# Kernel optimization log

Hardware: AMD Instinct MI355X
Metric: run time of the kernel (lower is better)

The kernel has to match this reference:

```python
import jax, jax.numpy as jnp
import numpy as np
import math

LMAX = 3
NUM_LAYERS = 2
MUL = 32
AVG_NEIGH = 16.0
CUTOFF = 2.5
P_ENV = 6
N_RB = 8

# ---------- real Clebsch-Gordan (Wigner 3j) coefficients ----------

def _su2_cg(j1, j2, j3, m1, m2, m3):
    if m1 + m2 != m3:
        return 0.0
    f = math.factorial
    pref = math.sqrt((2 * j3 + 1) * f(j1 + j2 - j3) * f(j1 - j2 + j3) * f(-j1 + j2 + j3) / f(j1 + j2 + j3 + 1)
                     * f(j3 + m3) * f(j3 - m3) * f(j1 - m1) * f(j1 + m1) * f(j2 - m2) * f(j2 + m2))
    s = 0.0
    kmin = max(0, j2 - j3 - m1, j1 - j3 + m2)
    kmax = min(j1 + j2 - j3, j1 - m1, j2 + m2)
    for k in range(kmin, kmax + 1):
        s += (-1.0) ** k / (f(k) * f(j1 + j2 - j3 - k) * f(j1 - m1 - k) * f(j2 + m2 - k)
                            * f(j3 - j2 + m1 + k) * f(j3 - j1 - m2 + k))
    return pref * s

def _q_real_to_complex(l):
    q = np.zeros((2 * l + 1, 2 * l + 1), dtype=np.complex128)
    for m in range(-l, 0):
        q[l + m, l + abs(m)] = 1 / np.sqrt(2)
        q[l + m, l - abs(m)] = -1j / np.sqrt(2)
    q[l, l] = 1.0
    for m in range(1, l + 1):
        q[l + m, l + abs(m)] = (-1) ** m / np.sqrt(2)
        q[l + m, l - abs(m)] = 1j * (-1) ** m / np.sqrt(2)
    return (-1j) ** l * q

def _real_cg(l1, l2, l3):
    C = np.zeros((2 * l1 + 1, 2 * l2 + 1, 2 * l3 + 1), dtype=np.complex128)
    for m1 in range(-l1, l1 + 1):
        for m2 in range(-l2, l2 + 1):
            m3 = m1 + m2
            if abs(m3) <= l3:
                C[l1 + m1, l2 + m2, l3 + m3] = _su2_cg(l1, l2, l3, m1, m2, m3)
    Q1, Q2, Q3 = _q_real_to_complex(l1), _q_real_to_complex(l2), _q_real_to_complex(l3)
    C = np.einsum('ia,jb,kc,abc->ijk', Q1, Q2, np.conj(Q3), C)
    Cr, Ci = np.real(C), np.imag(C)
    C = Cr if np.linalg.norm(Cr) >= np.linalg.norm(Ci) else Ci
    return (C / np.linalg.norm(C)).astype(np.float32)  # unit-norm invariant coupling tensor

W3J = {}
for _l1 in range(LMAX + 1):
    for _l2 in range(LMAX + 1):
        for _l3 in range(LMAX + 1):
            if abs(_l1 - _l2) <= _l3 <= _l1 + _l2:
                W3J[(_l1, _l2, _l3)] = jnp.asarray(_real_cg(_l1, _l2, _l3))

# ---------- spherical harmonics (component normalization, l=0..3) ----------

def _sh(u):
    x, y, z = u[:, 0], u[:, 1], u[:, 2]
    s3, s5, s15 = math.sqrt(3.0), math.sqrt(5.0), math.sqrt(15.0)
    sh0 = jnp.ones_like(x)[:, None]
    sh1 = s3 * jnp.stack([y, z, x], -1)
    sh2 = jnp.stack([s15 * x * y, s15 * y * z, 0.5 * s5 * (3 * z * z - 1.0),
                     s15 * x * z, 0.5 * s15 * (x * x - y * y)], -1)
    c1, c2, c3, c4 = math.sqrt(35.0 / 8.0), math.sqrt(105.0), math.sqrt(21.0 / 8.0), 0.5 * math.sqrt(7.0)
    sh3 = jnp.stack([c1 * y * (3 * x * x - y * y), c2 * x * y * z, c3 * y * (5 * z * z - 1.0),
                     c4 * z * (5 * z * z - 3.0), c3 * x * (5 * z * z - 1.0),
                     0.5 * c2 * z * (x * x - y * y), c1 * x * (x * x - 3 * y * y)], -1)
    return [sh0, sh1, sh2, sh3]

def _mlp(x, Ws):
    # e3nn-style MLP: no biases, 1/sqrt(fan_in) normalization, silu, linear last layer
    for i, W in enumerate(Ws):
        x = x @ (W / jnp.sqrt(1.0 * W.shape[0]))
        if i + 1 < len(Ws):
            x = jax.nn.silu(x)
    return x

def _envelope(x):
    p = P_ENV
    e = (1.0 - 0.5 * (p + 1) * (p + 2) * x ** p + p * (p + 2) * x ** (p + 1)
         - 0.5 * p * (p + 1) * x ** (p + 2))
    return jnp.where(x < 1.0, e, 0.0)

def _forward(node_attrs, vectors, we0, we1, winit, wenv, wlat0, wlat1, wmix, wout, senders, receivers):
    N = node_attrs.shape[0]
    E = vectors.shape[0]
    d = jnp.linalg.norm(vectors, axis=-1)                      # [E]
    uvec = vectors / (d[:, None] + 1e-9)                       # unit edge vectors
    dc = d / CUTOFF                                            # normalized distance in [0, inf)
    freqs = np.pi * np.arange(1, N_RB + 1, dtype=np.float32)
    rb = math.sqrt(2.0) * jnp.sin(dc[:, None] * freqs) / (dc[:, None] + 1e-9)  # [E, 8] Bessel basis
    cut = _envelope(dc)[:, None]                               # [E, 1] polynomial cutoff u(d, p)
    # two-body embedding: radial basis + sender/receiver species
    x = jnp.concatenate([rb, node_attrs[senders], node_attrs[receivers]], axis=-1)
    x = _mlp(x, [we0, we1]) * cut                              # [E, H]
    Y = _sh(uvec)                                              # list of [E, 2l+1]
    wi = (x @ (winit / jnp.sqrt(1.0 * winit.shape[0]))).reshape(E, LMAX + 1, MUL)
    V = [wi[:, l, :, None] * Y[l][:, None, :] for l in range(LMAX + 1)]  # [E, MUL, 2l+1]
    for layer in range(NUM_LAYERS):
        w = x @ (wenv[layer] / jnp.sqrt(1.0 * wenv.shape[1]))  # [E, MUL] env weights
        env = []
        for l in range(LMAX + 1):
            # environment embedding: scatter weighted SH onto nodes, gather back onto edges
            node_env = jax.ops.segment_sum(w[:, :, None] * Y[l][:, None, :], receivers, num_segments=N)
            env.append(node_env[senders] / jnp.sqrt(AVG_NEIGH))
        # equivariant CG tensor product env (x) V -> T, per output l3
        T = []
        for l3 in range(LMAX + 1):
            acc = None
            n = 0
            for l1 in range(LMAX + 1):
                for l2 in range(LMAX + 1):
                    if (l1, l2, l3) in W3J:
                        t = jnp.einsum('ijk,emi,emj->emk', W3J[(l1, l2, l3)], env[l1], V[l2])
                        acc = t if acc is None else acc + t
                        n += 1
            T.append(acc / np.sqrt(n))
        # scalars feed the latent track; latent MLP gated by cutoff
        x = jnp.concatenate([x, T[0][:, :, 0]], axis=-1)       # [E, H+MUL]
        x = _mlp(x, [wlat0[layer], wlat1[layer]]) * cut        # [E, H]
        # per-l channel mixing (e3nn Linear)
        V = [jnp.einsum('emk,mn->enk', T[l], wmix[layer, l] / jnp.sqrt(1.0 * MUL)) for l in range(LMAX + 1)]
    # output head: 0e per-edge scalar
    return x @ (wout / jnp.sqrt(1.0 * wout.shape[0]))          # [E, 1]

def setup_inputs():
    key = jax.random.key(0)
    ks = jax.random.split(key, 12)
    N, E, S, H = 4096, 65536, 16, 512
    L = NUM_LAYERS
    return {
        'node_attrs': jax.random.normal(ks[0], (N, S), jnp.float32),
        'vectors': jax.random.normal(ks[1], (E, 3), jnp.float32),
        'we0': jax.random.normal(ks[2], (N_RB + 2 * S, H), jnp.float32),
        'we1': jax.random.normal(ks[3], (H, H), jnp.float32),
        'winit': jax.random.normal(ks[4], (H, (LMAX + 1) * MUL), jnp.float32),
        'wenv': jax.random.normal(ks[5], (L, H, MUL), jnp.float32),
        'wlat0': jax.random.normal(ks[6], (L, H + MUL, H), jnp.float32),
        'wlat1': jax.random.normal(ks[7], (L, H, H), jnp.float32),
        'wmix': jax.random.normal(ks[8], (L, LMAX + 1, MUL, MUL), jnp.float32),
        'wout': jax.random.normal(ks[9], (H, 1), jnp.float32),
        'senders': jax.random.randint(ks[10], (E,), 0, N, jnp.int32),
        'receivers': jax.random.randint(ks[11], (E,), 0, N, jnp.int32),
    }

def reference(node_attrs, vectors, we0, we1, winit, wenv, wlat0, wlat1, wmix, wout, senders, receivers):
    return _forward(node_attrs, vectors, we0, we1, winit, wenv, wlat0, wlat1, wmix, wout, senders, receivers)
```

## Files before the change

### kernel.cpp

```cpp
#include <hip/hip_runtime.h>
#include <math.h>
#include <type_traits>

typedef __attribute__((ext_vector_type(8))) short s8v;
typedef __attribute__((ext_vector_type(4))) float f4v;
typedef __attribute__((ext_vector_type(2))) float f2v;

#define CH 8192

__device__ inline float b2f(unsigned short u){ return __uint_as_float(((unsigned)u)<<16); }
__device__ inline unsigned short f2b(float f){
  unsigned u = __float_as_uint(f);
  return (unsigned short)((u + 0x7FFFu + ((u>>16)&1u)) >> 16);
}
__device__ inline void stC(float* p, float v){ *p = v; }
__device__ inline void stC(unsigned short* p, float v){ *p = f2b(v); }

__device__ __forceinline__ void gl16(const void* g, void* l){
  __builtin_amdgcn_global_load_lds(
      (const __attribute__((address_space(1))) unsigned*)g,
      (__attribute__((address_space(3))) unsigned*)l, 16, 0, 0);
}

constexpr double FCT[11] = {1.,1.,2.,6.,24.,120.,720.,5040.,40320.,362880.,3628800.};
constexpr double csqrt_c(double x){
  double g = x > 1.0 ? x : 1.0;
  for (int i=0;i<60;i++) g = 0.5*(g + x/g);
  return g;
}
struct CD { double re, im; };
constexpr CD cmulc(CD a, CD b){ return {a.re*b.re - a.im*b.im, a.re*b.im + a.im*b.re}; }

constexpr double su2cg_c(int j1,int j2,int j3,int m1,int m2,int m3){
  if (m1+m2 != m3) return 0.0;
  double pref = csqrt_c((double)(2*j3+1) * FCT[j1+j2-j3]*FCT[j1-j2+j3]*FCT[-j1+j2+j3]/FCT[j1+j2+j3+1]
              * FCT[j3+m3]*FCT[j3-m3]*FCT[j1-m1]*FCT[j1+m1]*FCT[j2-m2]*FCT[j2+m2]);
  int kmin = 0;
  if (j2-j3-m1 > kmin) kmin = j2-j3-m1;
  if (j1-j3+m2 > kmin) kmin = j1-j3+m2;
  int kmax = j1+j2-j3;
  if (j1-m1 < kmax) kmax = j1-m1;
  if (j2+m2 < kmax) kmax = j2+m2;
  double s = 0.0;
  for (int k=kmin;k<=kmax;k++){
    double t = 1.0/(FCT[k]*FCT[j1+j2-j3-k]*FCT[j1-m1-k]*FCT[j2+m2-k]*FCT[j3-j2+m1+k]*FCT[j3-j1-m2+k]);
    s += (k&1) ? -t : t;
  }
  return pref*s;
}

constexpr CD qelem_c(int l, int i, int j){
  int m = i - l;
  const double is2 = 0.70710678118654752440;
  double re=0.0, im=0.0;
  if (m < 0){
    if (j == l - m) re = is2;
    else if (j == l + m) im = -is2;
  } else if (m == 0){
    if (j == l) re = 1.0;
  } else {
    double sgn = (m & 1) ? -1.0 : 1.0;
    if (j == l + m) re = sgn*is2;
    else if (j == l - m) im = sgn*is2;
  }
  CD r{};
  switch (l & 3){
    case 0: r = {re, im}; break;
    case 1: r = {im, -re}; break;
    case 2: r = {-re, -im}; break;
    default: r = {-im, re}; break;
  }
  return r;
}

constexpr double TN3[4] = {0.5, 1.0/3.0, 0.30151134457776363, 0.31622776601683794};

template<int L1,int L2,int L3>
struct TriVals { float v[(2*L1+1)*(2*L2+1)*(2*L3+1)]; };

template<int L1,int L2,int L3>
constexpr TriVals<L1,L2,L3> make_tri(){
  constexpr int n1=2*L1+1, n2=2*L2+1, n3=2*L3+1;
  double cg[n1*n2*n3] = {};
  for (int a=0;a<n1;a++)
    for (int b=0;b<n2;b++)
      for (int c=0;c<n3;c++)
        cg[(a*n2+b)*n3+c] = su2cg_c(L1,L2,L3, a-L1, b-L2, c-L3);
  double cr[n1*n2*n3] = {};
  double ci[n1*n2*n3] = {};
  for (int i=0;i<n1;i++)
   for (int j=0;j<n2;j++)
    for (int k=0;k<n3;k++){
      double sre=0.0, sim=0.0;
      for (int a=0;a<n1;a++){
        CD q1 = qelem_c(L1,i,a);
        if (q1.re==0.0 && q1.im==0.0) continue;
        for (int b=0;b<n2;b++){
          CD q2 = qelem_c(L2,j,b);
          if (q2.re==0.0 && q2.im==0.0) continue;
          CD q12 = cmulc(q1,q2);
          for (int c=0;c<n3;c++){
            double g = cg[(a*n2+b)*n3+c];
            if (g == 0.0) continue;
            CD q3 = qelem_c(L3,k,c);
            CD q3c{q3.re, -q3.im};
            CD q = cmulc(q12,q3c);
            sre += q.re*g; sim += q.im*g;
          }
        }
      }
      cr[(i*n2+j)*n3+k]=sre; ci[(i*n2+j)*n3+k]=sim;
    }
  double nr=0.0, ni=0.0;
  for (int i=0;i<n1*n2*n3;i++){ nr += cr[i]*cr[i]; ni += ci[i]*ci[i]; }
  bool pr = nr >= ni;
  double nn = csqrt_c(pr ? nr : ni);
  TriVals<L1,L2,L3> t{};
  for (int i=0;i<n1*n2*n3;i++)
    t.v[i] = (float)(((pr ? cr[i] : ci[i]) / nn) * TN3[L3]);
  return t;
}

template<int L1,int L2,int L3>
constexpr TriVals<L1,L2,L3> W3V = make_tri<L1,L2,L3>();

constexpr int LOFFC[4] = {0,1,4,9};

template<int WB>
__device__ __forceinline__ void fmac_lit(float& a, float p){
  asm("v_fmac_f32 %0, %2, %1" : "+v"(a) : "v"(p), "i"(WB));
}

template<int I, int N, typename F>
__device__ __forceinline__ void sfor(F&& f){
  if constexpr (I < N){
    f(std::integral_constant<int,I>{});
    sfor<I+1,N>(static_cast<F&&>(f));
  }
}

template<int L1,int L2>
__device__ __forceinline__ void tp_pair(const float* __restrict__ env,
                                        const float* __restrict__ v,
                                        float* __restrict__ acc){
  sfor<0,2*L1+1>([&](auto K1c){
    constexpr int k1 = decltype(K1c)::value;
    sfor<0,2*L2+1>([&](auto K2c){
      constexpr int k2 = decltype(K2c)::value;
      float p = env[LOFFC[L1]+k1] * v[LOFFC[L2]+k2];
      sfor<0,4>([&](auto L3c){
        constexpr int l3 = decltype(L3c)::value;
        constexpr int lo = (L1>L2)?(L1-L2):(L2-L1);
        if constexpr (l3 >= lo && l3 <= L1+L2){
          sfor<0,2*l3+1>([&](auto K3c){
            constexpr int k3 = decltype(K3c)::value;
            constexpr float w = W3V<L1,L2,l3>.v[(k1*(2*L2+1)+k2)*(2*l3+1)+k3];
            if constexpr (w != 0.f){
              fmac_lit<__builtin_bit_cast(int, w)>(acc[LOFFC[l3]+k3], p);
            }
          });
        }
      });
    });
  });
}

template<int L1,int L2,int L3>
__device__ __forceinline__ void tp_tri(const float* __restrict__ env,
                                       const float* __restrict__ v,
                                       float* __restrict__ acc){
  constexpr int n1=2*L1+1, n2=2*L2+1, n3=2*L3+1;
  #pragma unroll
  for (int k1=0;k1<n1;k1++)
    #pragma unroll
    for (int k2=0;k2<n2;k2++){
      float p = env[LOFFC[L1]+k1] * v[LOFFC[L2]+k2];
      #pragma unroll
      for (int k3=0;k3<n3;k3++){
        float w = W3V<L1,L2,L3>.v[(k1*n2+k2)*n3+k3];
        if (w != 0.f) acc[LOFFC[L3]+k3] += w * p;
      }
    }
}

struct WSeg { const float* W; unsigned short* WT; int K, N, Kpad, nblk; };
struct WDesc { WSeg s[9]; };
__global__ __launch_bounds__(256) void wconv_all(WDesc d){
  int b = blockIdx.x;
  int seg = 0;
  while (b >= d.s[seg].nblk){ b -= d.s[seg].nblk; ++seg; }
  const WSeg w = d.s[seg];
  int idx = b*256 + threadIdx.x;
  if (idx >= w.N*w.Kpad) return;
  int n = idx / w.Kpad, k = idx - n*w.Kpad;
  w.WT[idx] = (k < w.K) ? f2b(w.W[(size_t)k*w.N + n]) : (unsigned short)0;
}

__global__ __launch_bounds__(256) void edge_init(
    const float* __restrict__ vec, const float* __restrict__ na,
    const int* __restrict__ snd, const int* __restrict__ rcv,
    unsigned short* __restrict__ feat, float* __restrict__ Y, float* __restrict__ cutb, int E)
{
  int e = blockIdx.x*256 + threadIdx.x;
  if (e >= E) return;
  float vx = vec[(size_t)e*3], vy = vec[(size_t)e*3+1], vz = vec[(size_t)e*3+2];
  float d = sqrtf(vx*vx + vy*vy + vz*vz);
  float inv = 1.f/(d + 1e-9f);
  float x = vx*inv, y = vy*inv, z = vz*inv;
  float dc = d * 0.4f;
  float dci = 1.f/(dc + 1e-9f);
  unsigned short* f = feat + (size_t)e*64;
  #pragma unroll
  for (int k=1;k<=8;k++)
    f[k-1] = f2b(1.41421356237309515f * sinf(dc * 3.14159265358979323846f * k) * dci);
  int s = snd[e], r = rcv[e];
  #pragma unroll
  for (int i=0;i<16;i++) f[8+i]  = f2b(na[(size_t)s*16+i]);
  #pragma unroll
  for (int i=0;i<16;i++) f[24+i] = f2b(na[(size_t)r*16+i]);
  #pragma unroll
  for (int i=40;i<64;i++) f[i] = 0;
  float cv = 0.f;
  if (dc < 1.f){
    float d2 = dc*dc; float d6 = d2*d2*d2; float d7 = d6*dc; float d8 = d7*dc;
    cv = 1.f - 28.f*d6 + 48.f*d7 - 21.f*d8;
  }
  cutb[e] = cv;
  float* Ye = Y + (size_t)e*16;
  const float s3=1.7320508075688772f, s5=2.2360679774997896f, s15=3.8729833462074170f;
  Ye[0] = 1.f;
  Ye[1] = s3*y; Ye[2] = s3*z; Ye[3] = s3*x;
  Ye[4] = s15*x*y; Ye[5] = s15*y*z; Ye[6] = 0.5f*s5*(3.f*z*z-1.f);
  Ye[7] = s15*x*z; Ye[8] = 0.5f*s15*(x*x - y*y);
  const float c1=2.0916500663351889f, c2=10.246950765959598f, c3=1.6201851746019649f, c4=1.3228756555322954f;
  Ye[9]  = c1*y*(3.f*x*x - y*y);
  Ye[10] = c2*x*y*z;
  Ye[11] = c3*y*(5.f*z*z - 1.f);
  Ye[12] = c4*z*(5.f*z*z - 3.f);
  Ye[13] = c3*x*(5.f*z*z - 1.f);
  Ye[14] = 0.5f*c2*z*(x*x - y*y);
  Ye[15] = c1*x*(x*x - 3.f*y*y);
}

template<int NT, typename TC, bool SILU, bool CUT, bool HASA2>
__global__ __launch_bounds__(256) void gemm_mfma(
    const unsigned short* __restrict__ A, int lda, int K1,
    const float* __restrict__ A2, int lda2,
    const unsigned short* __restrict__ WT, int ldw,
    TC* __restrict__ C, int ldc,
    const float* __restrict__ cutv,
    int N, int K, float scale)
{
  constexpr int NB = NT/16;
  __shared__ s8v As8[128*8];
  __shared__ s8v Bs8[NT*8];
  const int tid = threadIdx.x;
  const int wid = tid >> 6, lane = tid & 63;
  const int r15 = lane & 15, kg = lane >> 4;
  const int col0 = blockIdx.x * NT;
  const int row0 = blockIdx.y * 128;
  f4v acc[2][NB] = {};

  auto compute = [&](){
    #pragma unroll
    for (int s = 0; s < 2; s++) {
      const int cb = s*4 + kg;
      const int cx = cb ^ (r15 & 7);
      s8v a0 = As8[(wid*32      + r15)*8 + cx];
      s8v a1 = As8[(wid*32 + 16 + r15)*8 + cx];
      #pragma unroll
      for (int j = 0; j < NB; j++) {
        s8v b = Bs8[(j*16 + r15)*8 + cx];
        acc[0][j] = __builtin_amdgcn_mfma_f32_16x16x32_bf16(a0, b, acc[0][j], 0,0,0);
        acc[1][j] = __builtin_amdgcn_mfma_f32_16x16x32_bf16(a1, b, acc[1][j], 0,0,0);
      }
    }
  };

  const int Kfull = HASA2 ? K1 : K;
  for (int k0 = 0; k0 < Kfull; k0 += 64) {
    #pragma unroll
    for (int i = 0; i < 4; i++) {
      int seg = i*256 + tid;
      int r = seg >> 3, ks = seg & 7;
      int ksx = ks ^ (r & 7);
      gl16(A + (size_t)(row0+r)*lda + k0 + ksx*8, &As8[i*256 + (tid & ~63)]);
    }
    #pragma unroll
    for (int i = 0; i < NT/32; i++) {
      int seg = i*256 + tid;
      int n = seg >> 3, ks = seg & 7;
      int ksx = ks ^ (n & 7);
      gl16(WT + (size_t)(col0+n)*ldw + k0 + ksx*8, &Bs8[i*256 + (tid & ~63)]);
    }
    __syncthreads();
    compute();
    __syncthreads();
  }
  if (HASA2 && Kfull < K) {
    #pragma unroll
    for (int i = 0; i < 4; i++) {
      int seg = i*256 + tid;
      int r = seg >> 3, ks = seg & 7;
      int cl = ks ^ (r & 7);
      s8v val = {};
      #pragma unroll
      for (int j = 0; j < 8; j++) {
        int kk = cl*8 + j;
        if (K1 + kk < K) val[j] = (short)f2b(A2[(size_t)(row0+r)*lda2 + kk]);
      }
      As8[seg] = val;
    }
    #pragma unroll
    for (int i = 0; i < NT/32; i++) {
      int seg = i*256 + tid;
      int n = seg >> 3, ks = seg & 7;
      int ksx = ks ^ (n & 7);
      gl16(WT + (size_t)(col0+n)*ldw + K1 + ksx*8, &Bs8[i*256 + (tid & ~63)]);
    }
    __syncthreads();
    compute();
  }
  #pragma unroll
  for (int g=0; g<2; g++) {
    #pragma unroll
    for (int c=0; c<NB; c++) {
      int col = col0 + c*16 + r15;
      if (col >= N) continue;
      #pragma unroll
      for (int j=0;j<4;j++) {
        int row = row0 + wid*32 + g*16 + kg*4 + j;
        float v = acc[g][c][j] * scale;
        if (SILU) v = v / (1.f + __expf(-v));
        if (CUT)  v *= cutv[row];
        stC(&C[(size_t)row*ldc + col], v);
      }
    }
  }
}

__global__ __launch_bounds__(256) void vbuild(
    const unsigned short* __restrict__ wi, const float* __restrict__ Y,
    unsigned short* __restrict__ V, int count)
{
  int t = blockIdx.x*256 + threadIdx.x;
  if (t >= count*32) return;
  int e = t >> 5, m = t & 31;
  const unsigned short* wr = wi + (size_t)e*128 + m;
  float ws[4] = { b2f(wr[0]), b2f(wr[32]), b2f(wr[64]), b2f(wr[96]) };
  const float4* Y4 = (const float4*)(Y + (size_t)e*16);
  float yv[16];
  #pragma unroll
  for (int q=0;q<4;q++){ float4 f=Y4[q]; yv[q*4]=f.x; yv[q*4+1]=f.y; yv[q*4+2]=f.z; yv[q*4+3]=f.w; }
  constexpr int LOFK[16] = {0,1,1,1,2,2,2,2,2,3,3,3,3,3,3,3};
  s8v o0, o1;
  #pragma unroll
  for (int k=0;k<8;k++)  o0[k] = (short)f2b(ws[LOFK[k]]   * yv[k]);
  #pragma unroll
  for (int k=0;k<8;k++)  o1[k] = (short)f2b(ws[LOFK[8+k]] * yv[8+k]);
  s8v* vo = (s8v*)(V + (size_t)e*512 + (size_t)m*16);
  vo[0] = o0; vo[1] = o1;
}

__global__ __launch_bounds__(256) void hist_k(
    const int* __restrict__ rcv, int* __restrict__ deg, int E)
{
  int e = blockIdx.x*256 + threadIdx.x;
  if (e < E) atomicAdd(&deg[rcv[e]], 1);
}

__global__ __launch_bounds__(256) void scan_k(
    const int* __restrict__ deg, int* __restrict__ offs, int Nn)
{
  __shared__ int part[256];
  const int t = threadIdx.x;
  const int per = (Nn + 255) / 256;
  int base = t*per;
  int loc[32];
  int s = 0;
  for (int i=0;i<per;i++){ int v = (base+i<Nn)?deg[base+i]:0; loc[i]=s; s+=v; }
  part[t] = s;
  __syncthreads();
  for (int off=1; off<256; off<<=1){
    int v = (t>=off) ? part[t-off] : 0;
    __syncthreads();
    part[t] += v;
    __syncthreads();
  }
  int pre = (t==0) ? 0 : part[t-1];
  for (int i=0;i<per;i++) if (base+i<Nn) offs[base+i] = pre + loc[i];
  if (t==255) offs[Nn] = part[255];
}

__global__ __launch_bounds__(256) void fill_k(
    const int* __restrict__ rcv, int* __restrict__ cursor,
    const int* __restrict__ offs, int* __restrict__ elist, int E)
{
  int e = blockIdx.x*256 + threadIdx.x;
  if (e >= E) return;
  int r = rcv[e];
  int p = atomicAdd(&cursor[r], 1);
  elist[offs[r] + p] = e;
}

__global__ __launch_bounds__(512) void env_build(
    const float* __restrict__ w, const float* __restrict__ Y,
    const int* __restrict__ elist, const int* __restrict__ offs,
    float* __restrict__ nenv)
{
  const int n = blockIdx.x;
  const int j = threadIdx.x;
  const int m = j >> 4, kk = j & 15;
  const int beg = offs[n], end = offs[n+1];
  float acc = 0.f;
  for (int p = beg; p < end; ++p) {
    int e = elist[p];
    acc += w[(size_t)e*32 + m] * Y[(size_t)e*16 + kk];
  }
  nenv[(size_t)n*512 + j] = acc;
}

__global__ __launch_bounds__(256, 2) void tp_mix(
    const float* __restrict__ nenv, const int* __restrict__ senders,
    unsigned short* __restrict__ V,
    const float* __restrict__ wm,
    float* __restrict__ t0, int E)
{
  __shared__ float Ts[8][32][18];
  const int tid = threadIdx.x;
  const int le = tid >> 5, m = tid & 31;
  const int e = blockIdx.x*8 + le;
  const int s = senders[e];
  float env[16], v[16], acc[16];
  const float4* ne4 = (const float4*)(nenv + (size_t)s*512 + (size_t)m*16);
  #pragma unroll
  for (int q=0;q<4;q++){
    float4 f = ne4[q];
    env[q*4]=f.x; env[q*4+1]=f.y; env[q*4+2]=f.z; env[q*4+3]=f.w;
  }
  const s8v* vv = (const s8v*)(V + (size_t)e*512 + (size_t)m*16);
  s8v v0 = vv[0], v1 = vv[1];
  #pragma unroll
  for (int q=0;q<8;q++){ v[q] = b2f((unsigned short)v0[q]); v[8+q] = b2f((unsigned short)v1[q]); }
  #pragma unroll
  for (int k=0;k<16;k++) acc[k] = 0.f;

  tp_pair<0,0>(env,v,acc); tp_pair<0,1>(env,v,acc); tp_pair<0,2>(env,v,acc); tp_pair<0,3>(env,v,acc);
  tp_pair<1,0>(env,v,acc); tp_pair<1,1>(env,v,acc); tp_pair<1,2>(env,v,acc); tp_pair<1,3>(env,v,acc);
  tp_pair<2,0>(env,v,acc); tp_pair<2,1>(env,v,acc); tp_pair<2,2>(env,v,acc); tp_pair<2,3>(env,v,acc);
  tp_pair<3,0>(env,v,acc); tp_pair<3,1>(env,v,acc); tp_pair<3,2>(env,v,acc); tp_pair<3,3>(env,v,acc);

  t0[(size_t)e*32 + m] = acc[0];

  #pragma unroll
  for (int k=0;k<16;k++) Ts[le][m][k] = acc[k];
  __syncthreads();
  f2v o2[8];
  #pragma unroll
  for (int kp=0;kp<8;kp++){ o2[kp][0]=0.f; o2[kp][1]=0.f; }
  #pragma unroll
  for (int mm=0; mm<32; mm++) {
    float w0 = wm[        mm*32 + m];
    float w1 = wm[1024 +  mm*32 + m];
    float w2 = wm[2048 +  mm*32 + m];
    float w3 = wm[3072 +  mm*32 + m];
    const f2v* tr = (const f2v*)Ts[le][mm];
    f2v p01; p01[0]=w0; p01[1]=w1;
    f2v p11; p11[0]=w1; p11[1]=w1;
    f2v p22; p22[0]=w2; p22[1]=w2;
    f2v p23; p23[0]=w2; p23[1]=w3;
    f2v p33; p33[0]=w3; p33[1]=w3;
    o2[0] += tr[0]*p01; o2[1] += tr[1]*p11; o2[2] += tr[2]*p22; o2[3] += tr[3]*p22;
    o2[4] += tr[4]*p23; o2[5] += tr[5]*p33; o2[6] += tr[6]*p33; o2[7] += tr[7]*p33;
  }
  s8v oa, ob;
  #pragma unroll
  for (int kp=0;kp<4;kp++){
    oa[2*kp]   = (short)f2b(o2[kp][0]   * 0.17677669529663689f);
    oa[2*kp+1] = (short)f2b(o2[kp][1]   * 0.17677669529663689f);
    ob[2*kp]   = (short)f2b(o2[4+kp][0] * 0.17677669529663689f);
    ob[2*kp+1] = (short)f2b(o2[4+kp][1] * 0.17677669529663689f);
  }
  s8v* vo = (s8v*)(V + (size_t)e*512 + (size_t)m*16);
  vo[0] = oa; vo[1] = ob;
}

__global__ __launch_bounds__(256) void tp_last(
    const float* __restrict__ nenv, const int* __restrict__ senders,
    const unsigned short* __restrict__ V, float* __restrict__ t0, int E)
{
  int t = blockIdx.x*256 + threadIdx.x;
  int e = t >> 5, m = t & 31;
  if (e >= E) return;
  int s = senders[e];
  float env[16], v[16], acc[16];
  const float4* ne4 = (const float4*)(nenv + (size_t)s*512 + (size_t)m*16);
  #pragma unroll
  for (int q=0;q<4;q++){
    float4 f = ne4[q];
    env[q*4]=f.x; env[q*4+1]=f.y; env[q*4+2]=f.z; env[q*4+3]=f.w;
  }
  const s8v* vv = (const s8v*)(V + (size_t)e*512 + (size_t)m*16);
  s8v v0 = vv[0], v1 = vv[1];
  #pragma unroll
  for (int q=0;q<8;q++){ v[q] = b2f((unsigned short)v0[q]); v[8+q] = b2f((unsigned short)v1[q]); }
  #pragma unroll
  for (int k=0;k<16;k++) acc[k] = 0.f;
  tp_tri<0,0,0>(env,v,acc); tp_tri<1,1,0>(env,v,acc);
  tp_tri<2,2,0>(env,v,acc); tp_tri<3,3,0>(env,v,acc);
  t0[(size_t)e*32 + m] = acc[0];
}

__global__ __launch_bounds__(256) void out_kernel(
    const unsigned short* __restrict__ x, const float* __restrict__ wout,
    float* __restrict__ out, int E)
{
  int gw = (blockIdx.x*256 + threadIdx.x) >> 6;
  int lane = threadIdx.x & 63;
  if (gw >= E) return;
  const s8v* xr = (const s8v*)(x + (size_t)gw*512);
  s8v chunk = xr[lane];
  float s = 0.f;
  #pragma unroll
  for (int j=0;j<8;j++) s += b2f((unsigned short)chunk[j]) * wout[lane*8 + j];
  #pragma unroll
  for (int off=32; off; off>>=1) s += __shfl_down(s, off);
  if (lane == 0) out[gw] = s * 0.044194173824159216f;
}

static inline size_t alup(size_t b){ return (b + 255) & ~(size_t)255; }
static size_t need_bytes(int E, int N, int chd){
  size_t s = 0;
  s += alup((size_t)E*16*4);
  s += alup((size_t)E*4);
  s += alup((size_t)E*32*4);
  s += alup((size_t)E*32*4);
  s += alup((size_t)N*512*4);
  s += alup((size_t)E*64*2);
  s += alup((size_t)chd*512*2);
  s += alup((size_t)E*512*2);
  s += alup((size_t)E*512*2);
  s += alup((size_t)512*64*2);
  s += alup((size_t)512*512*2);
  s += alup((size_t)128*512*2);
  s += alup((size_t)2*32*512*2);
  s += alup((size_t)2*512*544*2);
  s += alup((size_t)2*512*512*2);
  s += alup((size_t)N*4);
  s += alup(((size_t)N+1)*4);
  s += alup((size_t)N*4);
  s += alup((size_t)E*4);
  return s;
}

extern "C" void kernel_launch(void* const* d_in, const int* in_sizes, int n_in,
                              void* d_out, int out_size, void* d_ws, size_t ws_size,
                              hipStream_t stream)
{
  const float* node_attrs = (const float*)d_in[0];
  const float* vectors    = (const float*)d_in[1];
  const float* we0        = (const float*)d_in[2];
  const float* we1        = (const float*)d_in[3];
  const float* winit      = (const float*)d_in[4];
  const float* wenv       = (const float*)d_in[5];
  const float* wlat0      = (const float*)d_in[6];
  const float* wlat1      = (const float*)d_in[7];
  const float* wmix       = (const float*)d_in[8];
  const float* wout       = (const float*)d_in[9];
  const int*   senders    = (const int*)d_in[10];
  const int*   receivers  = (const int*)d_in[11];
  float* out = (float*)d_out;
  const int E = in_sizes[1] / 3;
  const int N = in_sizes[0] / 16;

  int CHD = -1;
  const int tiers[4] = {E, E/2, E/4, CH};
  for (int i=0;i<4;i++){
    if (tiers[i] >= CH && need_bytes(E, N, tiers[i]) <= ws_size){ CHD = tiers[i]; break; }
  }
  if (CHD < 0) return;

  char* base = (char*)d_ws;
  size_t off = 0;
  auto carve = [&](size_t b) -> char* { char* p = base + off; off += alup(b); return p; };
  float*          Yb    = (float*)carve((size_t)E*16*4);
  float*          cutb  = (float*)carve((size_t)E*4);
  float*          wbuf  = (float*)carve((size_t)E*32*4);
  float*          t0b   = (float*)carve((size_t)E*32*4);
  float*          nenv  = (float*)carve((size_t)N*512*4);
  unsigned short* feat  = (unsigned short*)carve((size_t)E*64*2);
  unsigned short* cbuf  = (unsigned short*)carve((size_t)CHD*512*2);
  unsigned short* Vb    = (unsigned short*)carve((size_t)E*512*2);
  unsigned short* xb    = (unsigned short*)carve((size_t)E*512*2);
  unsigned short* we0T  = (unsigned short*)carve((size_t)512*64*2);
  unsigned short* we1T  = (unsigned short*)carve((size_t)512*512*2);
  unsigned short* winT  = (unsigned short*)carve((size_t)128*512*2);
  unsigned short* wenvT = (unsigned short*)carve((size_t)2*32*512*2);
  unsigned short* wl0T  = (unsigned short*)carve((size_t)2*512*544*2);
  unsigned short* wl1T  = (unsigned short*)carve((size_t)2*512*512*2);
  int*            deg   = (int*)carve((size_t)N*4);
  int*            offs  = (int*)carve(((size_t)N+1)*4);
  int*            cursor= (int*)carve((size_t)N*4);
  int*            elist = (int*)carve((size_t)E*4);

  const float rs40  = 0.15811388300841897f;
  const float rs512 = 0.044194173824159216f;
  const float rs544 = 0.042874646285627205f;

  dim3 blk(256);
  WDesc wd;
  auto seg = [&](int i, const float* W, unsigned short* WT, int K, int Nn, int Kpad){
    wd.s[i] = { W, WT, K, Nn, Kpad, (Nn*Kpad + 255)/256 };
  };
  seg(0, we0,  we0T, 40, 512, 64);
  seg(1, we1,  we1T, 512, 512, 512);
  seg(2, winit, winT, 512, 128, 512);
  seg(3, wenv,                wenvT,            512, 32, 512);
  seg(4, wenv + (size_t)512*32, wenvT + (size_t)32*512, 512, 32, 512);
  seg(5, wlat0,                 wl0T,                 544, 512, 544);
  seg(6, wlat0 + (size_t)544*512, wl0T + (size_t)512*544, 544, 512, 544);
  seg(7, wlat1,                 wl1T,                 512, 512, 512);
  seg(8, wlat1 + (size_t)512*512, wl1T + (size_t)512*512, 512, 512, 512);
  int totblk = 0;
  for (int i=0;i<9;i++) totblk += wd.s[i].nblk;
  wconv_all<<<totblk, blk, 0, stream>>>(wd);

  edge_init<<<E/256, blk, 0, stream>>>(vectors, node_attrs, senders, receivers, feat, Yb, cutb, E);

  hipMemsetAsync(deg, 0, (size_t)N*4, stream);
  hipMemsetAsync(cursor, 0, (size_t)N*4, stream);
  hist_k<<<(E+255)/256, blk, 0, stream>>>(receivers, deg, E);
  scan_k<<<1, blk, 0, stream>>>(deg, offs, N);
  fill_k<<<(E+255)/256, blk, 0, stream>>>(receivers, cursor, offs, elist, E);

  for (int c0 = 0; c0 < E; c0 += CHD) {
    gemm_mfma<128,unsigned short,true,false,false><<<dim3(4, CHD/128), blk, 0, stream>>>(
        feat + (size_t)c0*64, 64, 64, nullptr, 0, we0T, 64, cbuf, 512, nullptr, 512, 64, rs40);
    gemm_mfma<128,unsigned short,false,true,false><<<dim3(4, CHD/128), blk, 0, stream>>>(
        cbuf, 512, 512, nullptr, 0, we1T, 512, xb + (size_t)c0*512, 512, cutb + c0, 512, 512, rs512);
    gemm_mfma<128,unsigned short,false,false,false><<<dim3(1, CHD/128), blk, 0, stream>>>(
        xb + (size_t)c0*512, 512, 512, nullptr, 0, winT, 512, cbuf, 128, nullptr, 128, 512, rs512);
    vbuild<<<(CHD*32)/256, blk, 0, stream>>>(cbuf, Yb + (size_t)c0*16, Vb + (size_t)c0*512, CHD);
  }

  for (int layer = 0; layer < 2; ++layer) {
    gemm_mfma<64,float,false,false,false><<<dim3(1, E/128), blk, 0, stream>>>(
        xb, 512, 512, nullptr, 0, wenvT + (size_t)layer*32*512, 512, wbuf, 32, nullptr, 32, 512, rs512*0.25f);
    env_build<<<N, 512, 0, stream>>>(wbuf, Yb, elist, offs, nenv);
    if (layer == 0)
      tp_mix<<<E/8, blk, 0, stream>>>(nenv, senders, Vb,
          wmix + (size_t)layer*4*32*32, t0b, E);
    else
      tp_last<<<(E*32)/256, blk, 0, stream>>>(nenv, senders, Vb, t0b, E);
    for (int c0 = 0; c0 < E; c0 += CHD) {
      gemm_mfma<128,unsigned short,true,false,true><<<dim3(4, CHD/128), blk, 0, stream>>>(
          xb + (size_t)c0*512, 512, 512, t0b + (size_t)c0*32, 32,
          wl0T + (size_t)layer*512*544, 544, cbuf, 512, nullptr, 512, 544, rs544);
      gemm_mfma<128,unsigned short,false,true,false><<<dim3(4, CHD/128), blk, 0, stream>>>(
          cbuf, 512, 512, nullptr, 0, wl1T + (size_t)layer*512*512, 512,
          xb + (size_t)c0*512, 512, cutb + c0, 512, 512, rs512);
    }
  }

  out_kernel<<<E/4, blk, 0, stream>>>(xb, wout, out, E);
}
```

Before: 715.3 us.

## Fold env and init projections into preceding GEMMs via precomposed weights

Precomputes the weight products we1·wenv, we1·winit and wlat1·wenv on device and appends them as extra output columns of the preceding GEMMs. The separate env-weight and init-projection GEMMs, which each re-read the full edge feature matrix, are eliminated. The edge buffer is widened to 672 columns so the env weights, init weights and t0 live beside the features, which also removes the fp32 A2 side path from the GEMM. The wmix table is pre-transposed and pre-scaled for vector loads. In exchange the folded weights are rounded to bf16 once as products rather than per stage, which changes rounding slightly, and the extra columns add some write traffic.

```diff
diff --git a/kernel.cpp b/kernel.cpp
--- a/kernel.cpp
+++ b/kernel.cpp
@@ -183,17 +183,31 @@
     }
 }
 
-struct WSeg { const float* W; unsigned short* WT; int K, N, Kpad, nblk; };
-struct WDesc { WSeg s[9]; };
+struct WSeg { const float* W; unsigned short* WT; int K, N, Kpad, nblk, trans; };
+struct WDesc { WSeg s[11]; };
 __global__ __launch_bounds__(256) void wconv_all(WDesc d){
   int b = blockIdx.x;
   int seg = 0;
   while (b >= d.s[seg].nblk){ b -= d.s[seg].nblk; ++seg; }
   const WSeg w = d.s[seg];
   int idx = b*256 + threadIdx.x;
-  if (idx >= w.N*w.Kpad) return;
-  int n = idx / w.Kpad, k = idx - n*w.Kpad;
-  w.WT[idx] = (k < w.K) ? f2b(w.W[(size_t)k*w.N + n]) : (unsigned short)0;
+  if (w.trans){
+    if (idx >= w.N*w.Kpad) return;
+    int n = idx / w.Kpad, k = idx - n*w.Kpad;
+    w.WT[idx] = (k < w.K) ? f2b(w.W[(size_t)k*w.N + n]) : (unsigned short)0;
+  } else {
+    if (idx >= w.K*w.N) return;
+    w.WT[idx] = f2b(w.W[idx]);
+  }
+}
+
+__global__ __launch_bounds__(256) void wmix_tr(
+    const float* __restrict__ wm, float* __restrict__ wmT)
+{
+  int idx = blockIdx.x*256 + threadIdx.x;
+  if (idx >= 4096) return;
+  int l = idx & 3, mm = (idx >> 2) & 31, m = idx >> 7;
+  wmT[idx] = wm[(size_t)l*1024 + mm*32 + m] * 0.17677669529663689f;
 }
 
 __global__ __launch_bounds__(256) void edge_init(
@@ -242,10 +256,9 @@
   Ye[15] = c1*x*(x*x - 3.f*y*y);
 }
 
-template<int NT, typename TC, bool SILU, bool CUT, bool HASA2>
+template<int NT, typename TC, bool SILU, bool CUT, bool TSTORE=false>
 __global__ __launch_bounds__(256) void gemm_mfma(
     const unsigned short* __restrict__ A, int lda, int K1,
-    const float* __restrict__ A2, int lda2,
     const unsigned short* __restrict__ WT, int ldw,
     TC* __restrict__ C, int ldc,
     const float* __restrict__ cutv,
@@ -277,8 +290,7 @@
     }
   };
 
-  const int Kfull = HASA2 ? K1 : K;
-  for (int k0 = 0; k0 < Kfull; k0 += 64) {
+  for (int k0 = 0; k0 < K; k0 += 64) {
     #pragma unroll
     for (int i = 0; i < 4; i++) {
       int seg = i*256 + tid;
@@ -297,30 +309,6 @@
     compute();
     __syncthreads();
   }
-  if (HASA2 && Kfull < K) {
-    #pragma unroll
-    for (int i = 0; i < 4; i++) {
-      int seg = i*256 + tid;
-      int r = seg >> 3, ks = seg & 7;
-      int cl = ks ^ (r & 7);
-      s8v val = {};
-      #pragma unroll
-      for (int j = 0; j < 8; j++) {
-        int kk = cl*8 + j;
-        if (K1 + kk < K) val[j] = (short)f2b(A2[(size_t)(row0+r)*lda2 + kk]);
-      }
-      As8[seg] = val;
-    }
-    #pragma unroll
-    for (int i = 0; i < NT/32; i++) {
-      int seg = i*256 + tid;
-      int n = seg >> 3, ks = seg & 7;
-      int ksx = ks ^ (n & 7);
-      gl16(WT + (size_t)(col0+n)*ldw + K1 + ksx*8, &Bs8[i*256 + (tid & ~63)]);
-    }
-    __syncthreads();
-    compute();
-  }
   #pragma unroll
   for (int g=0; g<2; g++) {
     #pragma unroll
@@ -333,20 +321,21 @@
         float v = acc[g][c][j] * scale;
         if (SILU) v = v / (1.f + __expf(-v));
         if (CUT)  v *= cutv[row];
-        stC(&C[(size_t)row*ldc + col], v);
+        if (TSTORE) stC(&C[(size_t)col*ldc + row], v);
+        else        stC(&C[(size_t)row*ldc + col], v);
       }
     }
   }
 }
 
 __global__ __launch_bounds__(256) void vbuild(
-    const unsigned short* __restrict__ wi, const float* __restrict__ Y,
+    const unsigned short* __restrict__ xbc, const float* __restrict__ Y,
     unsigned short* __restrict__ V, int count)
 {
   int t = blockIdx.x*256 + threadIdx.x;
   if (t >= count*32) return;
   int e = t >> 5, m = t & 31;
-  const unsigned short* wr = wi + (size_t)e*128 + m;
+  const unsigned short* wr = xbc + (size_t)e*672 + 544 + m;
   float ws[4] = { b2f(wr[0]), b2f(wr[32]), b2f(wr[64]), b2f(wr[96]) };
   const float4* Y4 = (const float4*)(Y + (size_t)e*16);
   float yv[16];
@@ -404,7 +393,7 @@
 }
 
 __global__ __launch_bounds__(512) void env_build(
-    const float* __restrict__ w, const float* __restrict__ Y,
+    const unsigned short* __restrict__ xb, const float* __restrict__ Y,
     const int* __restrict__ elist, const int* __restrict__ offs,
     float* __restrict__ nenv)
 {
@@ -415,7 +404,7 @@
   float acc = 0.f;
   for (int p = beg; p < end; ++p) {
     int e = elist[p];
-    acc += w[(size_t)e*32 + m] * Y[(size_t)e*16 + kk];
+    acc += b2f(xb[(size_t)e*672 + 512 + m]) * Y[(size_t)e*16 + kk];
   }
   nenv[(size_t)n*512 + j] = acc;
 }
@@ -423,8 +412,8 @@
 __global__ __launch_bounds__(256, 2) void tp_mix(
     const float* __restrict__ nenv, const int* __restrict__ senders,
     unsigned short* __restrict__ V,
-    const float* __restrict__ wm,
-    float* __restrict__ t0, int E)
+    const float* __restrict__ wmT,
+    unsigned short* __restrict__ xb, int E)
 {
   __shared__ float Ts[8][32][18];
   const int tid = threadIdx.x;
@@ -450,7 +439,7 @@
   tp_pair<2,0>(env,v,acc); tp_pair<2,1>(env,v,acc); tp_pair<2,2>(env,v,acc); tp_pair<2,3>(env,v,acc);
   tp_pair<3,0>(env,v,acc); tp_pair<3,1>(env,v,acc); tp_pair<3,2>(env,v,acc); tp_pair<3,3>(env,v,acc);
 
-  t0[(size_t)e*32 + m] = acc[0];
+  xb[(size_t)e*672 + 512 + m] = f2b(acc[0]);
 
   #pragma unroll
   for (int k=0;k<16;k++) Ts[le][m][k] = acc[k];
@@ -458,12 +447,11 @@
   f2v o2[8];
   #pragma unroll
   for (int kp=0;kp<8;kp++){ o2[kp][0]=0.f; o2[kp][1]=0.f; }
+  const float4* wrow = (const float4*)(wmT + (size_t)m*128);
   #pragma unroll
   for (int mm=0; mm<32; mm++) {
-    float w0 = wm[        mm*32 + m];
-    float w1 = wm[1024 +  mm*32 + m];
-    float w2 = wm[2048 +  mm*32 + m];
-    float w3 = wm[3072 +  mm*32 + m];
+    float4 wv = wrow[mm];
+    float w0=wv.x, w1=wv.y, w2=wv.z, w3=wv.w;
     const f2v* tr = (const f2v*)Ts[le][mm];
     f2v p01; p01[0]=w0; p01[1]=w1;
     f2v p11; p11[0]=w1; p11[1]=w1;
@@ -476,10 +464,10 @@
   s8v oa, ob;
   #pragma unroll
   for (int kp=0;kp<4;kp++){
-    oa[2*kp]   = (short)f2b(o2[kp][0]   * 0.17677669529663689f);
-    oa[2*kp+1] = (short)f2b(o2[kp][1]   * 0.17677669529663689f);
-    ob[2*kp]   = (short)f2b(o2[4+kp][0] * 0.17677669529663689f);
-    ob[2*kp+1] = (short)f2b(o2[4+kp][1] * 0.17677669529663689f);
+    oa[2*kp]   = (short)f2b(o2[kp][0]);
+    oa[2*kp+1] = (short)f2b(o2[kp][1]);
+    ob[2*kp]   = (short)f2b(o2[4+kp][0]);
+    ob[2*kp+1] = (short)f2b(o2[4+kp][1]);
   }
   s8v* vo = (s8v*)(V + (size_t)e*512 + (size_t)m*16);
   vo[0] = oa; vo[1] = ob;
@@ -487,7 +475,7 @@
 
 __global__ __launch_bounds__(256) void tp_last(
     const float* __restrict__ nenv, const int* __restrict__ senders,
-    const unsigned short* __restrict__ V, float* __restrict__ t0, int E)
+    const unsigned short* __restrict__ V, unsigned short* __restrict__ xb, int E)
 {
   int t = blockIdx.x*256 + threadIdx.x;
   int e = t >> 5, m = t & 31;
@@ -508,7 +496,7 @@
   for (int k=0;k<16;k++) acc[k] = 0.f;
   tp_tri<0,0,0>(env,v,acc); tp_tri<1,1,0>(env,v,acc);
   tp_tri<2,2,0>(env,v,acc); tp_tri<3,3,0>(env,v,acc);
-  t0[(size_t)e*32 + m] = acc[0];
+  xb[(size_t)e*672 + 512 + m] = f2b(acc[0]);
 }
 
 __global__ __launch_bounds__(256) void out_kernel(
@@ -518,7 +506,7 @@
   int gw = (blockIdx.x*256 + threadIdx.x) >> 6;
   int lane = threadIdx.x & 63;
   if (gw >= E) return;
-  const s8v* xr = (const s8v*)(x + (size_t)gw*512);
+  const s8v* xr = (const s8v*)(x + (size_t)gw*672);
   s8v chunk = xr[lane];
   float s = 0.f;
   #pragma unroll
@@ -533,19 +521,21 @@
   size_t s = 0;
   s += alup((size_t)E*16*4);
   s += alup((size_t)E*4);
-  s += alup((size_t)E*32*4);
-  s += alup((size_t)E*32*4);
   s += alup((size_t)N*512*4);
   s += alup((size_t)E*64*2);
   s += alup((size_t)chd*512*2);
   s += alup((size_t)E*512*2);
-  s += alup((size_t)E*512*2);
+  s += alup((size_t)E*672*2);
   s += alup((size_t)512*64*2);
-  s += alup((size_t)512*512*2);
+  s += alup((size_t)768*512*2);
   s += alup((size_t)128*512*2);
   s += alup((size_t)2*32*512*2);
-  s += alup((size_t)2*512*544*2);
-  s += alup((size_t)2*512*512*2);
+  s += alup((size_t)2*512*576*2);
+  s += alup((size_t)640*512*2);
+  s += alup((size_t)512*512*2);
+  s += alup((size_t)512*512*2);
+  s += alup((size_t)512*512*2);
+  s += alup(4096*4);
   s += alup((size_t)N*4);
   s += alup(((size_t)N+1)*4);
   s += alup((size_t)N*4);
@@ -585,19 +575,21 @@
   auto carve = [&](size_t b) -> char* { char* p = base + off; off += alup(b); return p; };
   float*          Yb    = (float*)carve((size_t)E*16*4);
   float*          cutb  = (float*)carve((size_t)E*4);
-  float*          wbuf  = (float*)carve((size_t)E*32*4);
-  float*          t0b   = (float*)carve((size_t)E*32*4);
   float*          nenv  = (float*)carve((size_t)N*512*4);
   unsigned short* feat  = (unsigned short*)carve((size_t)E*64*2);
   unsigned short* cbuf  = (unsigned short*)carve((size_t)CHD*512*2);
   unsigned short* Vb    = (unsigned short*)carve((size_t)E*512*2);
-  unsigned short* xb    = (unsigned short*)carve((size_t)E*512*2);
+  unsigned short* xb    = (unsigned short*)carve((size_t)E*672*2);
   unsigned short* we0T  = (unsigned short*)carve((size_t)512*64*2);
-  unsigned short* we1T  = (unsigned short*)carve((size_t)512*512*2);
+  unsigned short* weF   = (unsigned short*)carve((size_t)768*512*2);
   unsigned short* winT  = (unsigned short*)carve((size_t)128*512*2);
   unsigned short* wenvT = (unsigned short*)carve((size_t)2*32*512*2);
-  unsigned short* wl0T  = (unsigned short*)carve((size_t)2*512*544*2);
-  unsigned short* wl1T  = (unsigned short*)carve((size_t)2*512*512*2);
+  unsigned short* wl0T  = (unsigned short*)carve((size_t)2*512*576*2);
+  unsigned short* wl1F  = (unsigned short*)carve((size_t)640*512*2);
+  unsigned short* wl1T1 = (unsigned short*)carve((size_t)512*512*2);
+  unsigned short* we1c  = (unsigned short*)carve((size_t)512*512*2);
+  unsigned short* wl1c  = (unsigned short*)carve((size_t)512*512*2);
+  float*          wmT   = (float*)carve(4096*4);
   int*            deg   = (int*)carve((size_t)N*4);
   int*            offs  = (int*)carve(((size_t)N+1)*4);
   int*            cursor= (int*)carve((size_t)N*4);
@@ -609,21 +601,32 @@
 
   dim3 blk(256);
   WDesc wd;
-  auto seg = [&](int i, const float* W, unsigned short* WT, int K, int Nn, int Kpad){
-    wd.s[i] = { W, WT, K, Nn, Kpad, (Nn*Kpad + 255)/256 };
+  auto seg = [&](int i, const float* W, unsigned short* WT, int K, int Nn, int Kpad, int trans){
+    int elems = trans ? Nn*Kpad : K*Nn;
+    wd.s[i] = { W, WT, K, Nn, Kpad, (elems + 255)/256, trans };
   };
-  seg(0, we0,  we0T, 40, 512, 64);
-  seg(1, we1,  we1T, 512, 512, 512);
-  seg(2, winit, winT, 512, 128, 512);
-  seg(3, wenv,                wenvT,            512, 32, 512);
-  seg(4, wenv + (size_t)512*32, wenvT + (size_t)32*512, 512, 32, 512);
-  seg(5, wlat0,                 wl0T,                 544, 512, 544);
-  seg(6, wlat0 + (size_t)544*512, wl0T + (size_t)512*544, 544, 512, 544);
-  seg(7, wlat1,                 wl1T,                 512, 512, 512);
-  seg(8, wlat1 + (size_t)512*512, wl1T + (size_t)512*512, 512, 512, 512);
+  seg(0, we0,   we0T, 40, 512, 64, 1);
+  seg(1, we1,   weF,  512, 512, 512, 1);
+  seg(2, winit, winT, 512, 128, 512, 1);
+  seg(3, wenv,                  wenvT,                  512, 32, 512, 1);
+  seg(4, wenv + (size_t)512*32, wenvT + (size_t)32*512, 512, 32, 512, 1);
+  seg(5, wlat0,                   wl0T,                   544, 512, 576, 1);
+  seg(6, wlat0 + (size_t)544*512, wl0T + (size_t)512*576, 544, 512, 576, 1);
+  seg(7, wlat1,                   wl1F,  512, 512, 512, 1);
+  seg(8, wlat1 + (size_t)512*512, wl1T1, 512, 512, 512, 1);
+  seg(9, we1,   we1c, 512, 512, 512, 0);
+  seg(10, wlat1, wl1c, 512, 512, 512, 0);
   int totblk = 0;
-  for (int i=0;i<9;i++) totblk += wd.s[i].nblk;
+  for (int i=0;i<11;i++) totblk += wd.s[i].nblk;
   wconv_all<<<totblk, blk, 0, stream>>>(wd);
+  wmix_tr<<<16, blk, 0, stream>>>(wmix, wmT);
+
+  gemm_mfma<64,unsigned short,false,false,true><<<dim3(1,4), blk, 0, stream>>>(
+      we1c, 512, 512, wenvT, 512, weF + (size_t)512*512, 512, nullptr, 32, 512, rs512*0.25f);
+  gemm_mfma<128,unsigned short,false,false,true><<<dim3(1,4), blk, 0, stream>>>(
+      we1c, 512, 512, winT, 512, weF + (size_t)544*512, 512, nullptr, 128, 512, rs512);
+  gemm_mfma<64,unsigned short,false,false,true><<<dim3(1,4), blk, 0, stream>>>(
+      wl1c, 512, 512, wenvT + (size_t)32*512, 512, wl1F + (size_t)512*512, 512, nullptr, 32, 512, rs512*0.25f);
 
   edge_init<<<E/256, blk, 0, stream>>>(vectors, node_attrs, senders, receivers, feat, Yb, cutb, E);
 
@@ -634,31 +637,29 @@
   fill_k<<<(E+255)/256, blk, 0, stream>>>(receivers, cursor, offs, elist, E);
 
   for (int c0 = 0; c0 < E; c0 += CHD) {
-    gemm_mfma<128,unsigned short,true,false,false><<<dim3(4, CHD/128), blk, 0, stream>>>(
-        feat + (size_t)c0*64, 64, 64, nullptr, 0, we0T, 64, cbuf, 512, nullptr, 512, 64, rs40);
-    gemm_mfma<128,unsigned short,false,true,false><<<dim3(4, CHD/128), blk, 0, stream>>>(
-        cbuf, 512, 512, nullptr, 0, we1T, 512, xb + (size_t)c0*512, 512, cutb + c0, 512, 512, rs512);
-    gemm_mfma<128,unsigned short,false,false,false><<<dim3(1, CHD/128), blk, 0, stream>>>(
-        xb + (size_t)c0*512, 512, 512, nullptr, 0, winT, 512, cbuf, 128, nullptr, 128, 512, rs512);
-    vbuild<<<(CHD*32)/256, blk, 0, stream>>>(cbuf, Yb + (size_t)c0*16, Vb + (size_t)c0*512, CHD);
+    gemm_mfma<128,unsigned short,true,false><<<dim3(4, CHD/128), blk, 0, stream>>>(
+        feat + (size_t)c0*64, 64, 64, we0T, 64, cbuf, 512, nullptr, 512, 64, rs40);
+    gemm_mfma<128,unsigned short,false,true><<<dim3(6, CHD/128), blk, 0, stream>>>(
+        cbuf, 512, 512, weF, 512, xb + (size_t)c0*672, 672, cutb + c0, 672, 512, rs512);
+    vbuild<<<(CHD*32)/256, blk, 0, stream>>>(xb + (size_t)c0*672, Yb + (size_t)c0*16, Vb + (size_t)c0*512, CHD);
   }
 
   for (int layer = 0; layer < 2; ++layer) {
-    gemm_mfma<64,float,false,false,false><<<dim3(1, E/128), blk, 0, stream>>>(
-        xb, 512, 512, nullptr, 0, wenvT + (size_t)layer*32*512, 512, wbuf, 32, nullptr, 32, 512, rs512*0.25f);
-    env_build<<<N, 512, 0, stream>>>(wbuf, Yb, elist, offs, nenv);
+    env_build<<<N, 512, 0, stream>>>(xb, Yb, elist, offs, nenv);
     if (layer == 0)
-      tp_mix<<<E/8, blk, 0, stream>>>(nenv, senders, Vb,
-          wmix + (size_t)layer*4*32*32, t0b, E);
+      tp_mix<<<E/8, blk, 0, stream>>>(nenv, senders, Vb, wmT, xb, E);
     else
-      tp_last<<<(E*32)/256, blk, 0, stream>>>(nenv, senders, Vb, t0b, E);
+      tp_last<<<(E*32)/256, blk, 0, stream>>>(nenv, senders, Vb, xb, E);
     for (int c0 = 0; c0 < E; c0 += CHD) {
-      gemm_mfma<128,unsigned short,true,false,true><<<dim3(4, CHD/128), blk, 0, stream>>>(
-          xb + (size_t)c0*512, 512, 512, t0b + (size_t)c0*32, 32,
-          wl0T + (size_t)layer*512*544, 544, cbuf, 512, nullptr, 512, 544, rs544);
-      gemm_mfma<128,unsigned short,false,true,false><<<dim3(4, CHD/128), blk, 0, stream>>>(
-          cbuf, 512, 512, nullptr, 0, wl1T + (size_t)layer*512*512, 512,
-          xb + (size_t)c0*512, 512, cutb + c0, 512, 512, rs512);
+      gemm_mfma<128,unsigned short,true,false><<<dim3(4, CHD/128), blk, 0, stream>>>(
+          xb + (size_t)c0*672, 672, 576, wl0T + (size_t)layer*512*576, 576,
+          cbuf, 512, nullptr, 512, 576, rs544);
+      if (layer == 0)
+        gemm_mfma<128,unsigned short,false,true><<<dim3(5, CHD/128), blk, 0, stream>>>(
+            cbuf, 512, 512, wl1F, 512, xb + (size_t)c0*672, 672, cutb + c0, 544, 512, rs512);
+      else
+        gemm_mfma<128,unsigned short,false,true><<<dim3(4, CHD/128), blk, 0, stream>>>(
+            cbuf, 512, 512, wl1T1, 512, xb + (size_t)c0*672, 672, cutb + c0, 512, 512, rs512);
     }
   }
 
```

Measured after the change: 735.3 us. +2.8%, slower.
